# Performance work log

Measured on AMD Instinct MI355X. Metric: run time of the kernel, lower is better.

## Reference

```python
import jax, jax.numpy as jnp
import numpy as np

B, IN, H = 128, 512, 1024

def setup_inputs() -> dict:
    key = jax.random.key(0)
    ks = jax.random.split(key, 20)
    def lin(kw, kb, out_dim, in_dim):
        lim = 1.0 / np.sqrt(in_dim)
        W = jax.random.uniform(kw, (out_dim, in_dim), minval=-lim, maxval=lim)
        b = jax.random.uniform(kb, (out_dim,), minval=-lim, maxval=lim)
        return W, b
    W1, b1 = lin(ks[0], ks[1], H, IN)
    W2, b2 = lin(ks[2], ks[3], H, H)
    W3, b3 = lin(ks[4], ks[5], H, H)
    Wc, bc = lin(ks[6], ks[7], 1, H)
    Wr, br = lin(ks[8], ks[9], H, 1)
    Wn, bn = lin(ks[10], ks[11], 2, H)
    Wv, bv = lin(ks[12], ks[13], 1, H)
    alpha = 0.01 * (2.0 * jax.random.uniform(ks[14], (H, H)) - 1.0)
    items = jax.random.normal(ks[15], (B, IN))
    plastic_weights = jax.random.normal(ks[16], (B, H, H))
    reward = jax.random.normal(ks[17], (B, 1))
    return dict(items=items, plastic_weights=plastic_weights, reward=reward,
                W1=W1, b1=b1, W2=W2, b2=b2, W3=W3, b3=b3,
                Wc=Wc, bc=bc, Wr=Wr, br=br, Wn=Wn, bn=bn,
                alpha=alpha, Wv=Wv, bv=bv)

def reference(items, plastic_weights, reward, W1, b1, W2, b2, W3, b3,
              Wc, bc, Wr, br, Wn, bn, alpha, Wv, bv):
    # nonlinear item embeddings: [B, H]
    emb = jnp.tanh(items @ W1.T + b1)
    current = emb @ W2.T + b2  # [B, H]
    # elementwise-scaled batched GEMV: (alpha * plastic)[b,h,i] @ emb[b,i]
    plastic_contrib = jnp.einsum('bhi,bi->bh', alpha * plastic_weights, emb)
    pre_tanh_hidden = current + plastic_contrib
    hidden = jnp.tanh(pre_tanh_hidden)
    reward_emb = reward @ Wr.T + br  # [B, H]
    nm_out = jnp.tanh((jnp.tanh((hidden + reward_emb) @ W3.T + b3)) @ Wn.T + bn)  # [B, 2]
    neuromodulator = (nm_out[:, 0] - nm_out[:, 1])[:, None, None]  # [B,1,1]
    choice = jax.nn.sigmoid(hidden @ Wc.T + bc)  # [B, 1]
    value = hidden @ Wv.T + bv  # [B, 1]
    # Hebbian outer-product trace: [B, H, H]
    hebbian = jnp.tanh(jnp.einsum('bh,bi->bhi', pre_tanh_hidden, emb)) * 10.0
    new_plastic = jnp.clip(plastic_weights + neuromodulator * hebbian, -50.0, 50.0)
    return (choice, neuromodulator, value, new_plastic, hidden)
```

## Files before the change

kernel.cpp:

```cpp
#include <hip/hip_runtime.h>
#include <hip/hip_bf16.h>

#define BATCH 128
#define IN_DIM 512
#define HDIM 1024
#define BCHUNK 8

typedef __attribute__((ext_vector_type(4))) float f32x4;

__device__ __forceinline__ float fast_tanh(float x) {
    float e = __expf(2.0f * x);
    return 1.0f - 2.0f * __builtin_amdgcn_rcpf(e + 1.0f);
}

__global__ __launch_bounds__(256) void k1_emb(
    const float* __restrict__ items, const float* __restrict__ W1,
    const float* __restrict__ b1, float* __restrict__ emb_f)
{
    __shared__ float it[IN_DIM];
    int b = blockIdx.x, t = threadIdx.x;
    it[t] = items[b * IN_DIM + t];
    it[t + 256] = items[b * IN_DIM + t + 256];
    __syncthreads();
    #pragma unroll
    for (int j = 0; j < 4; ++j) {
        int h = t + 256 * j;
        const float* wrow = W1 + h * IN_DIM;
        float acc = 0.f;
        #pragma unroll 4
        for (int c = 0; c < IN_DIM; c += 4) {
            f32x4 w = *reinterpret_cast<const f32x4*>(wrow + c);
            acc += w[0] * it[c] + w[1] * it[c + 1] + w[2] * it[c + 2] + w[3] * it[c + 3];
        }
        emb_f[b * HDIM + h] = tanhf(acc + b1[h]);
    }
}

__global__ __launch_bounds__(256) void k2_hidden(
    const float* __restrict__ plastic, const float* __restrict__ alpha,
    const float* __restrict__ W2, const float* __restrict__ b2,
    const float* __restrict__ emb_f, float* __restrict__ pre_f, float* __restrict__ hid_f)
{
    int hg = blockIdx.x & 255;
    int bc = blockIdx.x >> 8;
    int w  = threadIdx.x >> 6;
    int l  = threadIdx.x & 63;
    int h  = (hg << 2) + w;

    const float* arow = alpha + (h << 10);
    const float* wrow = W2 + (h << 10);
    f32x4 ar[4], wr[4];
    #pragma unroll
    for (int c = 0; c < 4; ++c) {
        int i = c * 256 + l * 4;
        ar[c] = *reinterpret_cast<const f32x4*>(arow + i);
        wr[c] = *reinterpret_cast<const f32x4*>(wrow + i);
    }
    float b2h = b2[h];

    #pragma unroll 2
    for (int bb = 0; bb < BCHUNK; ++bb) {
        int b = bc * BCHUNK + bb;
        const float* prow = plastic + (((size_t)b) << 20) + ((size_t)h << 10);
        const float* erow = emb_f + (b << 10);
        float acc = 0.f;
        #pragma unroll
        for (int c = 0; c < 4; ++c) {
            int i = c * 256 + l * 4;
            f32x4 p = *reinterpret_cast<const f32x4*>(prow + i);
            f32x4 e = *reinterpret_cast<const f32x4*>(erow + i);
            acc += e[0] * fmaf(ar[c][0], p[0], wr[c][0]);
            acc += e[1] * fmaf(ar[c][1], p[1], wr[c][1]);
            acc += e[2] * fmaf(ar[c][2], p[2], wr[c][2]);
            acc += e[3] * fmaf(ar[c][3], p[3], wr[c][3]);
        }
        #pragma unroll
        for (int off = 32; off > 0; off >>= 1) acc += __shfl_xor(acc, off);
        if (l == 0) {
            float pre = acc + b2h;
            pre_f[(b << 10) + h] = pre;
            hid_f[(b << 10) + h] = tanhf(pre);
        }
    }
}

__global__ __launch_bounds__(256) void k3a_t3(
    const float* __restrict__ hid_f, const float* __restrict__ reward,
    const float* __restrict__ Wr, const float* __restrict__ br,
    const float* __restrict__ W3, const float* __restrict__ b3,
    float* __restrict__ t3_f)
{
    int bid = blockIdx.x;
    int b = bid >> 8;
    int h = ((bid & 255) << 2) + (threadIdx.x >> 6);
    int l = threadIdx.x & 63;
    float rw = reward[b];
    const float* wrow = W3 + (h << 10);
    const float* hrow = hid_f + (b << 10);
    float acc = 0.f;
    #pragma unroll
    for (int c = 0; c < 4; ++c) {
        int i = c * 256 + l * 4;
        f32x4 w  = *reinterpret_cast<const f32x4*>(wrow + i);
        f32x4 wr = *reinterpret_cast<const f32x4*>(Wr + i);
        f32x4 bb = *reinterpret_cast<const f32x4*>(br + i);
        f32x4 hh = *reinterpret_cast<const f32x4*>(hrow + i);
        #pragma unroll
        for (int j = 0; j < 4; ++j)
            acc += (hh[j] + fmaf(rw, wr[j], bb[j])) * w[j];
    }
    #pragma unroll
    for (int off = 32; off > 0; off >>= 1) acc += __shfl_xor(acc, off);
    if (l == 0) t3_f[(b << 10) + h] = tanhf(acc + b3[h]);
}

__global__ __launch_bounds__(256) void k3b_heads(
    const float* __restrict__ t3_f, const float* __restrict__ hid_f,
    const float* __restrict__ Wn, const float* __restrict__ bn,
    const float* __restrict__ Wc, const float* __restrict__ bc,
    const float* __restrict__ Wv, const float* __restrict__ bv,
    float* __restrict__ nm_f, float* __restrict__ out)
{
    int b = blockIdx.x, t = threadIdx.x;
    int w = t >> 6, l = t & 63;
    const float* src = (w < 2) ? (t3_f + (b << 10)) : (hid_f + (b << 10));
    const float* wv = (w == 0) ? Wn : (w == 1) ? (Wn + HDIM) : (w == 2) ? Wc : Wv;
    float acc = 0.f;
    #pragma unroll
    for (int c = 0; c < 4; ++c) {
        int i = c * 256 + l * 4;
        f32x4 wg = *reinterpret_cast<const f32x4*>(wv + i);
        f32x4 ss = *reinterpret_cast<const f32x4*>(src + i);
        acc += ss[0] * wg[0] + ss[1] * wg[1] + ss[2] * wg[2] + ss[3] * wg[3];
    }
    #pragma unroll
    for (int off = 32; off > 0; off >>= 1) acc += __shfl_xor(acc, off);
    __shared__ float red[4];
    if (l == 0) red[w] = acc;
    __syncthreads();
    if (t == 0) {
        float nm0 = tanhf(red[0] + bn[0]);
        float nm1 = tanhf(red[1] + bn[1]);
        float nm = nm0 - nm1;
        nm_f[b] = nm;
        out[BATCH + b] = nm;
        out[b] = 1.0f / (1.0f + __expf(-(red[2] + bc[0])));
        out[2 * BATCH + b] = red[3] + bv[0];
    }
    const size_t HID_OFF = (size_t)3 * BATCH + (size_t)BATCH * HDIM * HDIM;
    for (int i = t; i < HDIM; i += 256)
        out[HID_OFF + (size_t)b * HDIM + i] = hid_f[(b << 10) + i];
}

__global__ __launch_bounds__(256) void k4_update(
    const float* __restrict__ plastic, const float* __restrict__ emb_f,
    const float* __restrict__ pre_f, const float* __restrict__ nm_f,
    float* __restrict__ outp)
{
    const size_t NG = (size_t)BATCH * HDIM * HDIM / 4;
    size_t gid = (size_t)blockIdx.x * 256 + threadIdx.x;
    size_t idx = (NG - 1 - gid) * 4;
    int b   = (int)(idx >> 20);
    int rem = (int)(idx & 1048575u);
    int h   = rem >> 10;
    int i0  = rem & 1023;
    float nm  = nm_f[b];
    float pre = pre_f[(b << 10) + h];
    f32x4 p = *reinterpret_cast<const f32x4*>(plastic + idx);
    f32x4 e = *reinterpret_cast<const f32x4*>(emb_f + (b << 10) + i0);
    f32x4 o;
    #pragma unroll
    for (int j = 0; j < 4; ++j) {
        float heb = fast_tanh(pre * e[j]) * 10.0f;
        float v = fmaf(nm, heb, p[j]);
        o[j] = fminf(fmaxf(v, -50.0f), 50.0f);
    }
    __builtin_nontemporal_store(o, reinterpret_cast<f32x4*>(outp + idx));
}

extern "C" void kernel_launch(void* const* d_in, const int* in_sizes, int n_in,
                              void* d_out, int out_size, void* d_ws, size_t ws_size,
                              hipStream_t stream)
{
    const float* items   = (const float*)d_in[0];
    const float* plastic = (const float*)d_in[1];
    const float* reward  = (const float*)d_in[2];
    const float* W1 = (const float*)d_in[3];
    const float* b1 = (const float*)d_in[4];
    const float* W2 = (const float*)d_in[5];
    const float* b2 = (const float*)d_in[6];
    const float* W3 = (const float*)d_in[7];
    const float* b3 = (const float*)d_in[8];
    const float* Wc = (const float*)d_in[9];
    const float* bc = (const float*)d_in[10];
    const float* Wr = (const float*)d_in[11];
    const float* br = (const float*)d_in[12];
    const float* Wn = (const float*)d_in[13];
    const float* bn = (const float*)d_in[14];
    const float* alpha = (const float*)d_in[15];
    const float* Wv = (const float*)d_in[16];
    const float* bv = (const float*)d_in[17];

    float* ws    = (float*)d_ws;
    float* emb_f = ws;
    float* pre_f = ws + 131072;
    float* hid_f = ws + 262144;
    float* t3_f  = ws + 393216;
    float* nm_f  = ws + 524288;

    float* out  = (float*)d_out;
    float* outp = out + 384;

    k1_emb   <<<BATCH, 256, 0, stream>>>(items, W1, b1, emb_f);
    k2_hidden<<<(HDIM / 4) * (BATCH / BCHUNK), 256, 0, stream>>>(plastic, alpha, W2, b2, emb_f, pre_f, hid_f);
    k3a_t3   <<<(BATCH * HDIM) / 4, 256, 0, stream>>>(hid_f, reward, Wr, br, W3, b3, t3_f);
    k3b_heads<<<BATCH, 256, 0, stream>>>(t3_f, hid_f, Wn, bn, Wc, bc, Wv, bv, nm_f, out);
    k4_update<<<(size_t)(BATCH * HDIM) * HDIM / 1024, 256, 0, stream>>>(plastic, emb_f, pre_f, nm_f, outp);
}
```

Measured before the change: 406.7 us.

## Chunk batch through hidden/nm/update kernels so plastic reread hits cache

Splits the batch into chunks of 16 and, for each chunk, runs the hidden GEMV, the neuromodulator computation and the plastic update back to back, so the 64MB chunk of plastic weights read by k2 can still be resident in the large last-level cache when k4 rereads it. The neuromodulator projection is fused into the W3 kernel via per-block partial dot products with Wn accumulated by atomics, which removes the t3 buffer and a separate heads pass. The cost is many more kernel launches (three per chunk), smaller grids per launch with less parallelism, and float atomics whose summation order is nondeterministic.

```diff
diff --git a/kernel.cpp b/kernel.cpp
--- a/kernel.cpp
+++ b/kernel.cpp
@@ -4,7 +4,9 @@
 #define BATCH 128
 #define IN_DIM 512
 #define HDIM 1024
-#define BCHUNK 8
+#define CHUNK 16
+#define K2_BCHUNK 4
+#define K3_BCHUNK 8
 
 typedef __attribute__((ext_vector_type(4))) float f32x4;
 
@@ -15,10 +17,12 @@
 
 __global__ __launch_bounds__(256) void k1_emb(
     const float* __restrict__ items, const float* __restrict__ W1,
-    const float* __restrict__ b1, float* __restrict__ emb_f)
+    const float* __restrict__ b1, const float* __restrict__ bn,
+    float* __restrict__ emb_f, float* __restrict__ nm_acc)
 {
     __shared__ float it[IN_DIM];
     int b = blockIdx.x, t = threadIdx.x;
+    if (b == 0) nm_acc[t] = bn[t & 1];
     it[t] = items[b * IN_DIM + t];
     it[t + 256] = items[b * IN_DIM + t + 256];
     __syncthreads();
@@ -39,10 +43,11 @@
 __global__ __launch_bounds__(256) void k2_hidden(
     const float* __restrict__ plastic, const float* __restrict__ alpha,
     const float* __restrict__ W2, const float* __restrict__ b2,
-    const float* __restrict__ emb_f, float* __restrict__ pre_f, float* __restrict__ hid_f)
+    const float* __restrict__ emb_f, float* __restrict__ pre_f,
+    float* __restrict__ hid_f, int b0)
 {
     int hg = blockIdx.x & 255;
-    int bc = blockIdx.x >> 8;
+    int bg = blockIdx.x >> 8;
     int w  = threadIdx.x >> 6;
     int l  = threadIdx.x & 63;
     int h  = (hg << 2) + w;
@@ -59,8 +64,8 @@
     float b2h = b2[h];
 
     #pragma unroll 2
-    for (int bb = 0; bb < BCHUNK; ++bb) {
-        int b = bc * BCHUNK + bb;
+    for (int bb = 0; bb < K2_BCHUNK; ++bb) {
+        int b = b0 + bg * K2_BCHUNK + bb;
         const float* prow = plastic + (((size_t)b) << 20) + ((size_t)h << 10);
         const float* erow = emb_f + (b << 10);
         float acc = 0.f;
@@ -84,89 +89,75 @@
     }
 }
 
-__global__ __launch_bounds__(256) void k3a_t3(
+__global__ __launch_bounds__(256) void k3a_nm(
     const float* __restrict__ hid_f, const float* __restrict__ reward,
     const float* __restrict__ Wr, const float* __restrict__ br,
     const float* __restrict__ W3, const float* __restrict__ b3,
-    float* __restrict__ t3_f)
-{
-    int bid = blockIdx.x;
-    int b = bid >> 8;
-    int h = ((bid & 255) << 2) + (threadIdx.x >> 6);
-    int l = threadIdx.x & 63;
-    float rw = reward[b];
+    const float* __restrict__ Wn, float* __restrict__ nm_acc, int b0)
+{
+    int hg = blockIdx.x & 255;
+    int bg = blockIdx.x >> 8;
+    int w  = threadIdx.x >> 6;
+    int l  = threadIdx.x & 63;
+    int h  = (hg << 2) + w;
+
     const float* wrow = W3 + (h << 10);
-    const float* hrow = hid_f + (b << 10);
-    float acc = 0.f;
+    f32x4 w3r[4], wrr[4], brr[4];
     #pragma unroll
     for (int c = 0; c < 4; ++c) {
         int i = c * 256 + l * 4;
-        f32x4 w  = *reinterpret_cast<const f32x4*>(wrow + i);
-        f32x4 wr = *reinterpret_cast<const f32x4*>(Wr + i);
-        f32x4 bb = *reinterpret_cast<const f32x4*>(br + i);
-        f32x4 hh = *reinterpret_cast<const f32x4*>(hrow + i);
-        #pragma unroll
-        for (int j = 0; j < 4; ++j)
-            acc += (hh[j] + fmaf(rw, wr[j], bb[j])) * w[j];
-    }
-    #pragma unroll
-    for (int off = 32; off > 0; off >>= 1) acc += __shfl_xor(acc, off);
-    if (l == 0) t3_f[(b << 10) + h] = tanhf(acc + b3[h]);
-}
-
-__global__ __launch_bounds__(256) void k3b_heads(
-    const float* __restrict__ t3_f, const float* __restrict__ hid_f,
-    const float* __restrict__ Wn, const float* __restrict__ bn,
-    const float* __restrict__ Wc, const float* __restrict__ bc,
-    const float* __restrict__ Wv, const float* __restrict__ bv,
-    float* __restrict__ nm_f, float* __restrict__ out)
-{
-    int b = blockIdx.x, t = threadIdx.x;
-    int w = t >> 6, l = t & 63;
-    const float* src = (w < 2) ? (t3_f + (b << 10)) : (hid_f + (b << 10));
-    const float* wv = (w == 0) ? Wn : (w == 1) ? (Wn + HDIM) : (w == 2) ? Wc : Wv;
-    float acc = 0.f;
-    #pragma unroll
-    for (int c = 0; c < 4; ++c) {
-        int i = c * 256 + l * 4;
-        f32x4 wg = *reinterpret_cast<const f32x4*>(wv + i);
-        f32x4 ss = *reinterpret_cast<const f32x4*>(src + i);
-        acc += ss[0] * wg[0] + ss[1] * wg[1] + ss[2] * wg[2] + ss[3] * wg[3];
-    }
-    #pragma unroll
-    for (int off = 32; off > 0; off >>= 1) acc += __shfl_xor(acc, off);
-    __shared__ float red[4];
-    if (l == 0) red[w] = acc;
+        w3r[c] = *reinterpret_cast<const f32x4*>(wrow + i);
+        wrr[c] = *reinterpret_cast<const f32x4*>(Wr + i);
+        brr[c] = *reinterpret_cast<const f32x4*>(br + i);
+    }
+    float b3h = b3[h];
+    float wn0 = Wn[h], wn1 = Wn[HDIM + h];
+
+    __shared__ float part[4][K3_BCHUNK][2];
+
+    for (int bb = 0; bb < K3_BCHUNK; ++bb) {
+        int b = b0 + bg * K3_BCHUNK + bb;
+        float rw = reward[b];
+        const float* hrow = hid_f + (b << 10);
+        float acc = 0.f;
+        #pragma unroll
+        for (int c = 0; c < 4; ++c) {
+            int i = c * 256 + l * 4;
+            f32x4 hh = *reinterpret_cast<const f32x4*>(hrow + i);
+            #pragma unroll
+            for (int j = 0; j < 4; ++j)
+                acc += (hh[j] + fmaf(rw, wrr[c][j], brr[c][j])) * w3r[c][j];
+        }
+        #pragma unroll
+        for (int off = 32; off > 0; off >>= 1) acc += __shfl_xor(acc, off);
+        if (l == 0) {
+            float t3 = tanhf(acc + b3h);
+            part[w][bb][0] = t3 * wn0;
+            part[w][bb][1] = t3 * wn1;
+        }
+    }
     __syncthreads();
-    if (t == 0) {
-        float nm0 = tanhf(red[0] + bn[0]);
-        float nm1 = tanhf(red[1] + bn[1]);
-        float nm = nm0 - nm1;
-        nm_f[b] = nm;
-        out[BATCH + b] = nm;
-        out[b] = 1.0f / (1.0f + __expf(-(red[2] + bc[0])));
-        out[2 * BATCH + b] = red[3] + bv[0];
-    }
-    const size_t HID_OFF = (size_t)3 * BATCH + (size_t)BATCH * HDIM * HDIM;
-    for (int i = t; i < HDIM; i += 256)
-        out[HID_OFF + (size_t)b * HDIM + i] = hid_f[(b << 10) + i];
+    int t = threadIdx.x;
+    if (t < K3_BCHUNK * 2) {
+        int bb = t >> 1, j = t & 1;
+        float s = part[0][bb][j] + part[1][bb][j] + part[2][bb][j] + part[3][bb][j];
+        atomicAdd(nm_acc + ((b0 + bg * K3_BCHUNK + bb) << 1) + j, s);
+    }
 }
 
 __global__ __launch_bounds__(256) void k4_update(
     const float* __restrict__ plastic, const float* __restrict__ emb_f,
-    const float* __restrict__ pre_f, const float* __restrict__ nm_f,
-    float* __restrict__ outp)
-{
-    const size_t NG = (size_t)BATCH * HDIM * HDIM / 4;
-    size_t gid = (size_t)blockIdx.x * 256 + threadIdx.x;
-    size_t idx = (NG - 1 - gid) * 4;
+    const float* __restrict__ pre_f, const float* __restrict__ nm_acc,
+    float* __restrict__ outp, int b0)
+{
+    size_t idx = (((size_t)b0) << 20) + ((size_t)blockIdx.x * 256 + threadIdx.x) * 4;
     int b   = (int)(idx >> 20);
     int rem = (int)(idx & 1048575u);
     int h   = rem >> 10;
     int i0  = rem & 1023;
-    float nm  = nm_f[b];
+    float nm  = fast_tanh(nm_acc[2 * b]) - fast_tanh(nm_acc[2 * b + 1]);
     float pre = pre_f[(b << 10) + h];
-    f32x4 p = *reinterpret_cast<const f32x4*>(plastic + idx);
+    f32x4 p = __builtin_nontemporal_load(reinterpret_cast<const f32x4*>(plastic + idx));
     f32x4 e = *reinterpret_cast<const f32x4*>(emb_f + (b << 10) + i0);
     f32x4 o;
     #pragma unroll
@@ -176,6 +167,39 @@
         o[j] = fminf(fmaxf(v, -50.0f), 50.0f);
     }
     __builtin_nontemporal_store(o, reinterpret_cast<f32x4*>(outp + idx));
+}
+
+__global__ __launch_bounds__(256) void k3c_heads(
+    const float* __restrict__ hid_f, const float* __restrict__ nm_acc,
+    const float* __restrict__ Wc, const float* __restrict__ bc,
+    const float* __restrict__ Wv, const float* __restrict__ bv,
+    float* __restrict__ out)
+{
+    int b = blockIdx.x, t = threadIdx.x;
+    int w = t >> 6, l = t & 63;
+    const float* hrow = hid_f + (b << 10);
+    if (w < 2) {
+        const float* wv = (w == 0) ? Wc : Wv;
+        float acc = 0.f;
+        #pragma unroll
+        for (int c = 0; c < 4; ++c) {
+            int i = c * 256 + l * 4;
+            f32x4 wg = *reinterpret_cast<const f32x4*>(wv + i);
+            f32x4 ss = *reinterpret_cast<const f32x4*>(hrow + i);
+            acc += ss[0] * wg[0] + ss[1] * wg[1] + ss[2] * wg[2] + ss[3] * wg[3];
+        }
+        #pragma unroll
+        for (int off = 32; off > 0; off >>= 1) acc += __shfl_xor(acc, off);
+        if (l == 0) {
+            if (w == 0) out[b] = 1.0f / (1.0f + __expf(-(acc + bc[0])));
+            else        out[2 * BATCH + b] = acc + bv[0];
+        }
+    } else if (t == 128) {
+        out[BATCH + b] = tanhf(nm_acc[2 * b]) - tanhf(nm_acc[2 * b + 1]);
+    }
+    const size_t HID_OFF = (size_t)3 * BATCH + (size_t)BATCH * HDIM * HDIM;
+    for (int i = t; i < HDIM; i += 256)
+        out[HID_OFF + (size_t)b * HDIM + i] = hrow[i];
 }
 
 extern "C" void kernel_launch(void* const* d_in, const int* in_sizes, int n_in,
@@ -201,19 +225,25 @@
     const float* Wv = (const float*)d_in[16];
     const float* bv = (const float*)d_in[17];
 
-    float* ws    = (float*)d_ws;
-    float* emb_f = ws;
-    float* pre_f = ws + 131072;
-    float* hid_f = ws + 262144;
-    float* t3_f  = ws + 393216;
-    float* nm_f  = ws + 524288;
+    float* ws     = (float*)d_ws;
+    float* emb_f  = ws;
+    float* pre_f  = ws + 131072;
+    float* hid_f  = ws + 262144;
+    float* nm_acc = ws + 393216;
 
     float* out  = (float*)d_out;
     float* outp = out + 384;
 
-    k1_emb   <<<BATCH, 256, 0, stream>>>(items, W1, b1, emb_f);
-    k2_hidden<<<(HDIM / 4) * (BATCH / BCHUNK), 256, 0, stream>>>(plastic, alpha, W2, b2, emb_f, pre_f, hid_f);
-    k3a_t3   <<<(BATCH * HDIM) / 4, 256, 0, stream>>>(hid_f, reward, Wr, br, W3, b3, t3_f);
-    k3b_heads<<<BATCH, 256, 0, stream>>>(t3_f, hid_f, Wn, bn, Wc, bc, Wv, bv, nm_f, out);
-    k4_update<<<(size_t)(BATCH * HDIM) * HDIM / 1024, 256, 0, stream>>>(plastic, emb_f, pre_f, nm_f, outp);
-}
+    k1_emb<<<BATCH, 256, 0, stream>>>(items, W1, b1, bn, emb_f, nm_acc);
+
+    for (int b0 = 0; b0 < BATCH; b0 += CHUNK) {
+        k2_hidden<<<256 * (CHUNK / K2_BCHUNK), 256, 0, stream>>>(
+            plastic, alpha, W2, b2, emb_f, pre_f, hid_f, b0);
+        k3a_nm<<<256 * (CHUNK / K3_BCHUNK), 256, 0, stream>>>(
+            hid_f, reward, Wr, br, W3, b3, Wn, nm_acc, b0);
+        k4_update<<<(CHUNK << 20) / 1024, 256, 0, stream>>>(
+            plastic, emb_f, pre_f, nm_acc, outp, b0);
+    }
+
+    k3c_heads<<<BATCH, 256, 0, stream>>>(hid_f, nm_acc, Wc, bc, Wv, bv, out);
+}
```

New measurement: 441.2 us. +8.5%, slower.
